# Kernel tuning notes

Hardware: AMD Instinct MI355X
Metric: run time of the kernel (lower is better)

## Reference

```python
import jax, jax.numpy as jnp
import numpy as np

N, S, C, PE, E, L, H = 65536, 128, 128, 8, 262144, 3, 2
NT, ET = 120, 5
EPS_BN = 1e-5


def _bn(x, g, b):
    # training-mode BatchNorm1d over the node dimension
    m = x.mean(axis=0)
    v = x.var(axis=0)
    return (x - m) * jax.lax.rsqrt(v + EPS_BN) * g + b


def _forward(node_type, edge_index, edge_type, pe,
             pe_gamma, pe_beta, pe_W, pe_b, node_emb, edge_emb,
             gine_W1, gine_b1, gine_W2, gine_b2,
             n1_g, n1_b, n2_g, n2_b, n3_g, n3_b,
             attn_inW, attn_inb, attn_outW, attn_outb,
             mlp_W1, mlp_b1, mlp_W2, mlp_b2):
    # input features: [node-type embedding | Linear(BN(pe))]  -> [N, C]
    x = jnp.concatenate([node_emb[node_type],
                         _bn(pe, pe_gamma, pe_beta) @ pe_W + pe_b], axis=1)
    ea = edge_emb[edge_type]            # [E, C], shared across layers
    src, dst = edge_index[0], edge_index[1]
    B = N // S                          # equal-size graphs -> dense batch is a reshape
    hd = C // H
    scale = 1.0 / np.sqrt(hd).astype(np.float32)
    for l in range(L):
        # --- GINEConv (eps=0): gather -> relu(x_j + e_ij) -> scatter-sum -> MLP ---
        msg = jax.nn.relu(x[src] + ea)                       # [E, C]
        agg = jax.ops.segment_sum(msg, dst, num_segments=N)  # [N, C]
        z = x + agg
        h = jax.nn.relu(z @ gine_W1[l] + gine_b1[l]) @ gine_W2[l] + gine_b2[l]
        h = _bn(h + x, n1_g[l], n1_b[l])                     # local branch + residual + BN
        # --- global multi-head self-attention within each graph ---
        xb = x.reshape(B, S, C)
        qkv = xb @ attn_inW[l] + attn_inb[l]                 # [B, S, 3C]
        q, k, v = jnp.split(qkv, 3, axis=-1)
        q = q.reshape(B, S, H, hd)
        k = k.reshape(B, S, H, hd)
        v = v.reshape(B, S, H, hd)
        att = jax.nn.softmax(jnp.einsum('bqhd,bkhd->bhqk', q, k) * scale, axis=-1)
        o = jnp.einsum('bhqk,bkhd->bqhd', att, v).reshape(B, S, C)
        o = (o @ attn_outW[l] + attn_outb[l]).reshape(N, C)
        ha = _bn(o + x, n2_g[l], n2_b[l])                    # attn branch + residual + BN
        # --- combine + FFN ---
        out = h + ha
        out = out + (jax.nn.relu(out @ mlp_W1[l] + mlp_b1[l]) @ mlp_W2[l] + mlp_b2[l])
        x = _bn(out, n3_g[l], n3_b[l])
    return x


def setup_inputs() -> dict:
    keys = iter(jax.random.split(jax.random.key(0), 40))
    nk = lambda: next(keys)
    p = lambda *s: jax.random.normal(nk(), s, jnp.float32) * 0.05
    return {
        'node_type': jax.random.randint(nk(), (N,), 0, NT),
        'pe': jax.random.normal(nk(), (N, 20), jnp.float32),
        'edge_index': jax.random.randint(nk(), (2, E), 0, N),
        'edge_type': jax.random.randint(nk(), (E,), 0, ET),
        'batch': jnp.arange(N) // S,   # 512 equal-size graphs of 128 nodes
        'pe_gamma': jnp.ones(20), 'pe_beta': jnp.zeros(20),
        'pe_W': p(20, PE), 'pe_b': jnp.zeros(PE),
        'node_emb': p(NT, C - PE), 'edge_emb': p(ET, C),
        'gine_W1': p(L, C, C), 'gine_b1': jnp.zeros((L, C)),
        'gine_W2': p(L, C, C), 'gine_b2': jnp.zeros((L, C)),
        'n1_g': jnp.ones((L, C)), 'n1_b': jnp.zeros((L, C)),
        'n2_g': jnp.ones((L, C)), 'n2_b': jnp.zeros((L, C)),
        'n3_g': jnp.ones((L, C)), 'n3_b': jnp.zeros((L, C)),
        'attn_inW': p(L, C, 3 * C), 'attn_inb': jnp.zeros((L, 3 * C)),
        'attn_outW': p(L, C, C), 'attn_outb': jnp.zeros((L, C)),
        'mlp_W1': p(L, C, 2 * C), 'mlp_b1': jnp.zeros((L, 2 * C)),
        'mlp_W2': p(L, 2 * C, C), 'mlp_b2': jnp.zeros((L, C)),
    }


def reference(node_type, pe, edge_index, edge_type, batch,
              pe_gamma, pe_beta, pe_W, pe_b, node_emb, edge_emb,
              gine_W1, gine_b1, gine_W2, gine_b2,
              n1_g, n1_b, n2_g, n2_b, n3_g, n3_b,
              attn_inW, attn_inb, attn_outW, attn_outb,
              mlp_W1, mlp_b1, mlp_W2, mlp_b2):
    # 'batch' is implicit via the equal-size-graph reshape in _forward
    return _forward(node_type, edge_index, edge_type, pe,
                    pe_gamma, pe_beta, pe_W, pe_b, node_emb, edge_emb,
                    gine_W1, gine_b1, gine_W2, gine_b2,
                    n1_g, n1_b, n2_g, n2_b, n3_g, n3_b,
                    attn_inW, attn_inb, attn_outW, attn_outb,
                    mlp_W1, mlp_b1, mlp_W2, mlp_b2)
```

## Files before the change

kernel.cpp:

```cpp
#include <hip/hip_runtime.h>
#include <hip/hip_bf16.h>

#define NN 65536
#define SS 128
#define CC 128
#define EE 262144
#define BB 512
#define LL 3
#define NREP 64

typedef __attribute__((ext_vector_type(8))) short bf16x8;
typedef __attribute__((ext_vector_type(4))) float f32x4;

__device__ __forceinline__ float b2f(unsigned short u) {
    union { unsigned int i; float f; } x; x.i = ((unsigned int)u) << 16; return x.f;
}
__device__ __forceinline__ unsigned short f2b(float f) {
    union { float f; unsigned int i; } x; x.f = f;
    unsigned int r = x.i + 0x7fffu + ((x.i >> 16) & 1u);
    return (unsigned short)(r >> 16);
}
#define SWB(row, colbyte, ROWB) ((row) * (ROWB) + ((colbyte) ^ (((row) & 7) << 4)))

__global__ __launch_bounds__(256) void hist_k(const int* __restrict__ eidx, int* __restrict__ cnt) {
    const int e = blockIdx.x * 256 + threadIdx.x;
    atomicAdd(&cnt[eidx[EE + e]], 1);
}
__global__ __launch_bounds__(256) void scan1_k(const int* __restrict__ cnt, int* __restrict__ row,
                                               int* __restrict__ part) {
    __shared__ int s[256];
    const int tid = threadIdx.x;
    const int i = blockIdx.x * 256 + tid;
    const int v = cnt[i];
    s[tid] = v;
    __syncthreads();
    for (int off = 1; off < 256; off <<= 1) {
        int t = (tid >= off) ? s[tid - off] : 0;
        __syncthreads(); s[tid] += t; __syncthreads();
    }
    row[i] = s[tid] - v;
    if (tid == 255) part[blockIdx.x] = s[255];
}
__global__ __launch_bounds__(256) void scan2_k(int* __restrict__ part) {
    __shared__ int s[256];
    const int tid = threadIdx.x;
    const int v = part[tid];
    s[tid] = v;
    __syncthreads();
    for (int off = 1; off < 256; off <<= 1) {
        int t = (tid >= off) ? s[tid - off] : 0;
        __syncthreads(); s[tid] += t; __syncthreads();
    }
    part[tid] = s[tid] - v;
}
__global__ __launch_bounds__(256) void scan3_k(int* __restrict__ row, const int* __restrict__ part) {
    const int i = blockIdx.x * 256 + threadIdx.x;
    row[i] += part[blockIdx.x];
    if (i == 0) row[NN] = EE;
}
__global__ __launch_bounds__(256) void fill_k(const int* __restrict__ eidx, const int* __restrict__ row,
                                              int* __restrict__ cnt, int* __restrict__ elist) {
    const int e = blockIdx.x * 256 + threadIdx.x;
    const int d = eidx[EE + e];
    const int slot = row[d] + atomicAdd(&cnt[d], 1);
    elist[slot] = e;
}

__global__ __launch_bounds__(256) void cvtw(const float* __restrict__ gW1, const float* __restrict__ gW2,
                                            const float* __restrict__ inW, const float* __restrict__ oW,
                                            const float* __restrict__ mW1, const float* __restrict__ mW2,
                                            unsigned short* __restrict__ WB) {
    const int g = blockIdx.x * 256 + threadIdx.x;
    const int l = g / 163840;
    const int r = g % 163840;
    const float* src; int K, Nc, dst, i;
    if (r < 16384)       { src = gW1 + l * 16384; K = 128; Nc = 128; dst = 0;      i = r; }
    else if (r < 32768)  { src = gW2 + l * 16384; K = 128; Nc = 128; dst = 16384;  i = r - 16384; }
    else if (r < 81920)  { src = inW + l * 49152; K = 128; Nc = 384; dst = 32768;  i = r - 32768; }
    else if (r < 98304)  { src = oW  + l * 16384; K = 128; Nc = 128; dst = 81920;  i = r - 81920; }
    else if (r < 131072) { src = mW1 + l * 32768; K = 128; Nc = 256; dst = 98304;  i = r - 98304; }
    else                 { src = mW2 + l * 32768; K = 256; Nc = 128; dst = 131072; i = r - 131072; }
    const int k = i / Nc, c = i % Nc;
    WB[(size_t)l * 163840 + dst + (size_t)c * K + k] = f2b(src[i]);
}

__global__ __launch_bounds__(256) void colstats_pe(const float* __restrict__ pe,
                                                   float* __restrict__ stats) {
    const int r = blockIdx.x * 256 + threadIdx.x;
    const float* p = pe + (size_t)r * 20;
    float v[20];
    *(float4*)&v[0]  = *(const float4*)(p);
    *(float4*)&v[4]  = *(const float4*)(p + 4);
    *(float4*)&v[8]  = *(const float4*)(p + 8);
    *(float4*)&v[12] = *(const float4*)(p + 12);
    *(float4*)&v[16] = *(const float4*)(p + 16);
    float s[20], q[20];
#pragma unroll
    for (int i = 0; i < 20; ++i) { s[i] = v[i]; q[i] = v[i] * v[i]; }
#pragma unroll
    for (int off = 1; off < 64; off <<= 1) {
#pragma unroll
        for (int i = 0; i < 20; ++i) {
            s[i] += __shfl_xor(s[i], off);
            q[i] += __shfl_xor(q[i], off);
        }
    }
    __shared__ float red[4][40];
    const int lane = threadIdx.x & 63, w = threadIdx.x >> 6;
    if (lane == 0) {
#pragma unroll
        for (int i = 0; i < 20; ++i) { red[w][i] = s[i]; red[w][20 + i] = q[i]; }
    }
    __syncthreads();
    if (threadIdx.x < 40) {
        const float t = red[0][threadIdx.x] + red[1][threadIdx.x] +
                        red[2][threadIdx.x] + red[3][threadIdx.x];
        atomicAdd(&stats[threadIdx.x], t);
    }
}

__global__ void bn_finalize(const float* __restrict__ stats, const float* __restrict__ g,
                            const float* __restrict__ b, float* __restrict__ scoff,
                            int ncols, float invn, int nrep) {
    const int c = threadIdx.x;
    if (c < ncols) {
        float s = 0.f, q = 0.f;
#pragma unroll 8
        for (int r = 0; r < nrep; ++r) {
            s += stats[r * 2 * ncols + c];
            q += stats[r * 2 * ncols + ncols + c];
        }
        float m = s * invn;
        float var = q * invn - m * m;
        float rs = rsqrtf(var + 1e-5f);
        float sc = g[c] * rs;
        scoff[c] = sc;
        scoff[ncols + c] = b[c] - m * sc;
    }
}
__global__ __launch_bounds__(256) void bn_apply_b(const float* __restrict__ in,
                                                  const float* __restrict__ scoff,
                                                  unsigned short* __restrict__ out) {
    const size_t g = (size_t)blockIdx.x * 256 + threadIdx.x;
    const int c8 = ((int)g & 15) << 3;
    float4 a0 = *(const float4*)(in + g * 8);
    float4 a1 = *(const float4*)(in + g * 8 + 4);
    float v[8] = {a0.x, a0.y, a0.z, a0.w, a1.x, a1.y, a1.z, a1.w};
    union { uint4 u; unsigned short s[8]; } o;
#pragma unroll
    for (int i = 0; i < 8; ++i) o.s[i] = f2b(v[i] * scoff[c8 + i] + scoff[128 + c8 + i]);
    *(uint4*)(out + g * 8) = o.u;
}
__global__ __launch_bounds__(256) void bn_apply_f(const float* __restrict__ in,
                                                  const float* __restrict__ scoff,
                                                  float* __restrict__ out) {
    const size_t g = (size_t)blockIdx.x * 256 + threadIdx.x;
    const int c8 = ((int)g & 15) << 3;
    float4 a0 = *(const float4*)(in + g * 8);
    float4 a1 = *(const float4*)(in + g * 8 + 4);
    float v[8] = {a0.x, a0.y, a0.z, a0.w, a1.x, a1.y, a1.z, a1.w};
    float4 o0, o1;
    o0.x = v[0] * scoff[c8 + 0] + scoff[128 + c8 + 0];
    o0.y = v[1] * scoff[c8 + 1] + scoff[128 + c8 + 1];
    o0.z = v[2] * scoff[c8 + 2] + scoff[128 + c8 + 2];
    o0.w = v[3] * scoff[c8 + 3] + scoff[128 + c8 + 3];
    o1.x = v[4] * scoff[c8 + 4] + scoff[128 + c8 + 4];
    o1.y = v[5] * scoff[c8 + 5] + scoff[128 + c8 + 5];
    o1.z = v[6] * scoff[c8 + 6] + scoff[128 + c8 + 6];
    o1.w = v[7] * scoff[c8 + 7] + scoff[128 + c8 + 7];
    *(float4*)(out + g * 8) = o0;
    *(float4*)(out + g * 8 + 4) = o1;
}
__global__ __launch_bounds__(256) void combine2(const float* __restrict__ z,
                                                const float* __restrict__ ha,
                                                const float* __restrict__ scoff,
                                                unsigned short* __restrict__ out) {
    const size_t g = (size_t)blockIdx.x * 256 + threadIdx.x;
    const int c8 = ((int)g & 15) << 3;
    float4 a0 = *(const float4*)(z + g * 8);
    float4 a1 = *(const float4*)(z + g * 8 + 4);
    float4 b0 = *(const float4*)(ha + g * 8);
    float4 b1 = *(const float4*)(ha + g * 8 + 4);
    float va[8] = {a0.x, a0.y, a0.z, a0.w, a1.x, a1.y, a1.z, a1.w};
    float vb[8] = {b0.x, b0.y, b0.z, b0.w, b1.x, b1.y, b1.z, b1.w};
    union { uint4 u; unsigned short s[8]; } o;
#pragma unroll
    for (int i = 0; i < 8; ++i) {
        const int c = c8 + i;
        o.s[i] = f2b(va[i] * scoff[c] + scoff[128 + c] +
                     vb[i] * scoff[256 + c] + scoff[384 + c]);
    }
    *(uint4*)(out + g * 8) = o.u;
}

__global__ __launch_bounds__(256) void embed_b(const int* __restrict__ node_type,
                                               const float* __restrict__ pe,
                                               const float* __restrict__ scoff,
                                               const float* __restrict__ peW,
                                               const float* __restrict__ peB,
                                               const float* __restrict__ node_emb,
                                               unsigned short* __restrict__ XB) {
    const int g = blockIdx.x * 256 + threadIdx.x;
    const int n = g >> 4, c8 = (g & 15) << 3;
    float v[8];
    if (c8 < 120) {
        const float4 a = *(const float4*)(node_emb + (size_t)node_type[n] * 120 + c8);
        const float4 b = *(const float4*)(node_emb + (size_t)node_type[n] * 120 + c8 + 4);
        v[0] = a.x; v[1] = a.y; v[2] = a.z; v[3] = a.w;
        v[4] = b.x; v[5] = b.y; v[6] = b.z; v[7] = b.w;
    } else {
#pragma unroll
        for (int j = 0; j < 8; ++j) v[j] = peB[j];
#pragma unroll
        for (int k = 0; k < 20; ++k) {
            const float p = pe[(size_t)n * 20 + k] * scoff[k] + scoff[20 + k];
#pragma unroll
            for (int j = 0; j < 8; ++j) v[j] = fmaf(p, peW[k * 8 + j], v[j]);
        }
    }
    union { uint4 u; unsigned short s[8]; } o;
#pragma unroll
    for (int i = 0; i < 8; ++i) o.s[i] = f2b(v[i]);
    *(uint4*)(XB + (size_t)g * 8) = o.u;
}

__global__ __launch_bounds__(256) void gine_gather_b(const unsigned short* __restrict__ XB,
                                                     const int* __restrict__ eidx,
                                                     const int* __restrict__ etype,
                                                     const float* __restrict__ edge_emb,
                                                     const int* __restrict__ row,
                                                     const int* __restrict__ elist,
                                                     unsigned short* __restrict__ Z) {
    const int n = blockIdx.x * 16 + (threadIdx.x >> 4);
    const int c8 = (threadIdx.x & 15) << 3;
    const int beg = row[n], end = row[n + 1];
    union { uint4 u; unsigned short s[8]; } x;
    x.u = *(const uint4*)(XB + (size_t)n * 128 + c8);
    float z[8];
#pragma unroll
    for (int i = 0; i < 8; ++i) z[i] = b2f(x.s[i]);
    for (int j = beg; j < end; ++j) {
        const int e = elist[j];
        const int s = eidx[e];
        const int et = etype[e];
        union { uint4 u; unsigned short s[8]; } xs;
        xs.u = *(const uint4*)(XB + (size_t)s * 128 + c8);
        const float4 e0 = *(const float4*)(edge_emb + (size_t)et * 128 + c8);
        const float4 e1 = *(const float4*)(edge_emb + (size_t)et * 128 + c8 + 4);
        z[0] += fmaxf(b2f(xs.s[0]) + e0.x, 0.f);
        z[1] += fmaxf(b2f(xs.s[1]) + e0.y, 0.f);
        z[2] += fmaxf(b2f(xs.s[2]) + e0.z, 0.f);
        z[3] += fmaxf(b2f(xs.s[3]) + e0.w, 0.f);
        z[4] += fmaxf(b2f(xs.s[4]) + e1.x, 0.f);
        z[5] += fmaxf(b2f(xs.s[5]) + e1.y, 0.f);
        z[6] += fmaxf(b2f(xs.s[6]) + e1.z, 0.f);
        z[7] += fmaxf(b2f(xs.s[7]) + e1.w, 0.f);
    }
    union { uint4 u; unsigned short s[8]; } o;
#pragma unroll
    for (int i = 0; i < 8; ++i) o.s[i] = f2b(z[i]);
    *(uint4*)(Z + (size_t)n * 128 + c8) = o.u;
}

template <int RELU, int RESID, int STATS, int KS, int OUTF>
__global__ __launch_bounds__(256) void gemm_ls(const unsigned short* __restrict__ A,
                                               const unsigned short* __restrict__ WT,
                                               const float* __restrict__ bias,
                                               const unsigned short* __restrict__ resid,
                                               void* __restrict__ outp,
                                               float* __restrict__ stats, int Nw) {
    extern __shared__ __align__(16) char LDSX[];
    const int K = KS * 32;
    const int ROWB = K * 2;
    const int tid = threadIdx.x, lane = tid & 63, w = tid >> 6;
    const int lr = lane & 15, lg = lane >> 4;
    const int bm = blockIdx.x * 128;
    const int bn = blockIdx.y * 128;

#pragma unroll
    for (int i = 0; i < K / 16; ++i) {
        const int c = (i * 256 + tid) * 16;
        const int row = c / ROWB, inrow = c % ROWB;
        *(uint4*)(LDSX + SWB(row, inrow, ROWB)) =
            *(const uint4*)(WT + (size_t)(bn + row) * K + (inrow >> 1));
    }
    bf16x8 af[2][KS];
#pragma unroll
    for (int r = 0; r < 2; ++r)
#pragma unroll
        for (int ks = 0; ks < KS; ++ks)
            af[r][ks] = *(const bf16x8*)(A + (size_t)(bm + w * 32 + r * 16 + lr) * K + ks * 32 + lg * 8);
    float bcol[8];
#pragma unroll
    for (int nt = 0; nt < 8; ++nt) bcol[nt] = bias[bn + nt * 16 + lr];
    __syncthreads();

    f32x4 acc[2][8];
#pragma unroll
    for (int r = 0; r < 2; ++r)
#pragma unroll
        for (int nt = 0; nt < 8; ++nt) acc[r][nt] = (f32x4){0.f, 0.f, 0.f, 0.f};
#pragma unroll
    for (int ks = 0; ks < KS; ++ks) {
        bf16x8 bq[8];
#pragma unroll
        for (int nt = 0; nt < 8; ++nt)
            bq[nt] = *(const bf16x8*)(LDSX + SWB(nt * 16 + lr, ks * 64 + lg * 16, ROWB));
#pragma unroll
        for (int r = 0; r < 2; ++r)
#pragma unroll
            for (int nt = 0; nt < 8; ++nt)
                acc[r][nt] = __builtin_amdgcn_mfma_f32_16x16x32_bf16(af[r][ks], bq[nt], acc[r][nt], 0, 0, 0);
    }
    __syncthreads();

#pragma unroll
    for (int r = 0; r < 2; ++r)
#pragma unroll
        for (int nt = 0; nt < 8; ++nt)
#pragma unroll
            for (int j = 0; j < 4; ++j) {
                float v = acc[r][nt][j] + bcol[nt];
                if (RELU) v = fmaxf(v, 0.f);
                const int rl = w * 32 + r * 16 + lg * 4 + j;
                const int col = nt * 16 + lr;
                if (OUTF) ((float*)LDSX)[rl * 128 + col] = v;
                else ((unsigned short*)LDSX)[rl * 128 + col] = f2b(v);
            }
    __syncthreads();

    if (OUTF) {
        float ssum[4] = {0.f, 0.f, 0.f, 0.f}, ssq[4] = {0.f, 0.f, 0.f, 0.f};
#pragma unroll
        for (int i = 0; i < 16; ++i) {
            const int L = (i * 256 + tid) * 16;
            const int row = L >> 9, col = (L & 511) >> 2;
            float4 v = *(const float4*)(LDSX + L);
            if (RESID) {
                const uint2 rv = *(const uint2*)(resid + (size_t)(bm + row) * Nw + bn + col);
                v.x += b2f((unsigned short)(rv.x & 0xffffu));
                v.y += b2f((unsigned short)(rv.x >> 16));
                v.z += b2f((unsigned short)(rv.y & 0xffffu));
                v.w += b2f((unsigned short)(rv.y >> 16));
            }
            if (STATS) {
                ssum[0] += v.x; ssq[0] += v.x * v.x;
                ssum[1] += v.y; ssq[1] += v.y * v.y;
                ssum[2] += v.z; ssq[2] += v.z * v.z;
                ssum[3] += v.w; ssq[3] += v.w * v.w;
            }
            *(float4*)((float*)outp + (size_t)(bm + row) * Nw + bn + col) = v;
        }
        if (STATS) {
#pragma unroll
            for (int c2 = 0; c2 < 4; ++c2) {
                ssum[c2] += __shfl_xor(ssum[c2], 32);
                ssq[c2]  += __shfl_xor(ssq[c2], 32);
            }
            if (lane < 32) {
                float* st = stats + (size_t)(blockIdx.x & (NREP - 1)) * 256;
                const int c0 = (lane & 31) * 4;
#pragma unroll
                for (int c2 = 0; c2 < 4; ++c2) {
                    atomicAdd(&st[c0 + c2], ssum[c2]);
                    atomicAdd(&st[128 + c0 + c2], ssq[c2]);
                }
            }
        }
    } else {
#pragma unroll
        for (int i = 0; i < 8; ++i) {
            const int L = (i * 256 + tid) * 16;
            const int row = L >> 8, colb = L & 255;
            *(uint4*)((char*)outp + ((size_t)(bm + row) * Nw + bn) * 2 + colb) = *(const uint4*)(LDSX + L);
        }
    }
}

__global__ __launch_bounds__(256) void attn_mfma(const unsigned short* __restrict__ R,
                                                 unsigned short* __restrict__ O) {
    __shared__ __align__(16) unsigned short SH[128 * 128];
    __shared__ __align__(16) unsigned short Vp[128 * 72];
    __shared__ float inv[128];
    const int b = blockIdx.x >> 1, h = blockIdx.x & 1;
    const int tid = threadIdx.x, lane = tid & 63, w = tid >> 6;
    const int lr = lane & 15, lg = lane >> 4;
    unsigned short* Qs = SH;
    unsigned short* Ks = SH + 128 * 64;
    const size_t rb = (size_t)b * 128 * 384 + h * 64;
#pragma unroll
    for (int i = 0; i < 4; ++i) {
        const int f = tid + i * 256;
        const int r = f >> 3, ch = f & 7;
        *(uint4*)((char*)Qs + SWB(r, ch * 16, 128)) = *(const uint4*)(R + rb + (size_t)r * 384 + ch * 8);
        *(uint4*)((char*)Ks + SWB(r, ch * 16, 128)) = *(const uint4*)(R + rb + (size_t)r * 384 + 128 + ch * 8);
        *(uint4*)((char*)Vp + r * 144 + ch * 16) = *(const uint4*)(R + rb + (size_t)r * 384 + 256 + ch * 8);
    }
    __syncthreads();
    f32x4 s[8][2];
#pragma unroll
    for (int m = 0; m < 8; ++m)
#pragma unroll
        for (int n = 0; n < 2; ++n) s[m][n] = (f32x4){0.f, 0.f, 0.f, 0.f};
#pragma unroll
    for (int kd = 0; kd < 2; ++kd) {
        bf16x8 ak[8], bq[2];
#pragma unroll
        for (int m = 0; m < 8; ++m)
            ak[m] = *(const bf16x8*)((const char*)Ks + SWB(m * 16 + lr, kd * 64 + lg * 16, 128));
#pragma unroll
        for (int n = 0; n < 2; ++n)
            bq[n] = *(const bf16x8*)((const char*)Qs + SWB(w * 32 + n * 16 + lr, kd * 64 + lg * 16, 128));
#pragma unroll
        for (int m = 0; m < 8; ++m)
#pragma unroll
            for (int n = 0; n < 2; ++n)
                s[m][n] = __builtin_amdgcn_mfma_f32_16x16x32_bf16(ak[m], bq[n], s[m][n], 0, 0, 0);
    }
    const float SC = 0.125f * 1.44269504f;
#pragma unroll
    for (int n = 0; n < 2; ++n) {
        float mx = -1e30f;
#pragma unroll
        for (int m = 0; m < 8; ++m)
#pragma unroll
            for (int j = 0; j < 4; ++j) { s[m][n][j] *= SC; mx = fmaxf(mx, s[m][n][j]); }
        mx = fmaxf(mx, __shfl_xor(mx, 16));
        mx = fmaxf(mx, __shfl_xor(mx, 32));
        float sum = 0.f;
#pragma unroll
        for (int m = 0; m < 8; ++m)
#pragma unroll
            for (int j = 0; j < 4; ++j) {
                const float p = exp2f(s[m][n][j] - mx);
                s[m][n][j] = p;
                sum += p;
            }
        sum += __shfl_xor(sum, 16);
        sum += __shfl_xor(sum, 32);
        if (lg == 0) inv[w * 32 + n * 16 + lr] = 1.0f / sum;
    }
    __syncthreads();
#pragma unroll
    for (int n = 0; n < 2; ++n) {
        const int q = w * 32 + n * 16 + lr;
#pragma unroll
        for (int m = 0; m < 8; ++m) {
            ushort4 pk;
            pk.x = f2b(s[m][n][0]); pk.y = f2b(s[m][n][1]);
            pk.z = f2b(s[m][n][2]); pk.w = f2b(s[m][n][3]);
            *(ushort4*)((char*)SH + SWB(q, (m * 16 + lg * 4) * 2, 256)) = pk;
        }
    }
    __syncthreads();
    f32x4 o[2][4];
#pragma unroll
    for (int m = 0; m < 2; ++m)
#pragma unroll
        for (int n = 0; n < 4; ++n) o[m][n] = (f32x4){0.f, 0.f, 0.f, 0.f};
#pragma unroll
    for (int ks = 0; ks < 4; ++ks) {
        bf16x8 ap[2], bv[4];
#pragma unroll
        for (int m = 0; m < 2; ++m)
            ap[m] = *(const bf16x8*)((const char*)SH + SWB(w * 32 + m * 16 + lr, ks * 64 + lg * 16, 256));
#pragma unroll
        for (int n = 0; n < 4; ++n) {
            union { bf16x8 v; unsigned short u[8]; } t;
#pragma unroll
            for (int i = 0; i < 8; ++i) t.u[i] = Vp[(ks * 32 + lg * 8 + i) * 72 + n * 16 + lr];
            bv[n] = t.v;
        }
#pragma unroll
        for (int m = 0; m < 2; ++m)
#pragma unroll
            for (int n = 0; n < 4; ++n)
                o[m][n] = __builtin_amdgcn_mfma_f32_16x16x32_bf16(ap[m], bv[n], o[m][n], 0, 0, 0);
    }
    __syncthreads();
    unsigned short* Os = SH;
#pragma unroll
    for (int m = 0; m < 2; ++m)
#pragma unroll
        for (int j = 0; j < 4; ++j) {
            const int q = w * 32 + m * 16 + lg * 4 + j;
            const float sc = inv[q];
#pragma unroll
            for (int n = 0; n < 4; ++n)
                Os[q * 64 + n * 16 + lr] = f2b(o[m][n][j] * sc);
        }
    __syncthreads();
#pragma unroll
    for (int i = 0; i < 4; ++i) {
        const int L = (i * 256 + tid) * 16;
        const int row = L >> 7, colb = L & 127;
        *(uint4*)((char*)O + ((size_t)(b * 128 + row) * 128 + h * 64) * 2 + colb) =
            *(const uint4*)((const char*)Os + L);
    }
}

extern "C" void kernel_launch(void* const* d_in, const int* in_sizes, int n_in,
                              void* d_out, int out_size, void* d_ws, size_t ws_size,
                              hipStream_t stream) {
    const int* node_type = (const int*)d_in[0];
    const float* pe = (const float*)d_in[1];
    const int* eidx = (const int*)d_in[2];
    const int* etype = (const int*)d_in[3];
    const float* pe_gamma = (const float*)d_in[5];
    const float* pe_beta = (const float*)d_in[6];
    const float* pe_W = (const float*)d_in[7];
    const float* pe_b = (const float*)d_in[8];
    const float* node_emb = (const float*)d_in[9];
    const float* edge_emb = (const float*)d_in[10];
    const float* gine_W1 = (const float*)d_in[11];
    const float* gine_b1 = (const float*)d_in[12];
    const float* gine_W2 = (const float*)d_in[13];
    const float* gine_b2 = (const float*)d_in[14];
    const float* n1_g = (const float*)d_in[15];
    const float* n1_b = (const float*)d_in[16];
    const float* n2_g = (const float*)d_in[17];
    const float* n2_b = (const float*)d_in[18];
    const float* n3_g = (const float*)d_in[19];
    const float* n3_b = (const float*)d_in[20];
    const float* attn_inW = (const float*)d_in[21];
    const float* attn_inb = (const float*)d_in[22];
    const float* attn_outW = (const float*)d_in[23];
    const float* attn_outb = (const float*)d_in[24];
    const float* mlp_W1 = (const float*)d_in[25];
    const float* mlp_b1 = (const float*)d_in[26];
    const float* mlp_W2 = (const float*)d_in[27];
    const float* mlp_b2 = (const float*)d_in[28];

    const size_t NC = (size_t)NN * CC;
    unsigned short* XB = (unsigned short*)d_ws;
    unsigned short* Zb = XB + NC;
    unsigned short* T1 = Zb + NC;
    unsigned short* Rq = T1 + NC;
    float* HAf = (float*)Rq;
    unsigned short* OUTb = Rq + 2 * NC;
    unsigned short* T2 = Rq + 3 * NC;
    float* Zf = (float*)(T2 + 2 * NC);
    unsigned short* WB = (unsigned short*)(Zf + NC);
    float* STATS = (float*)(WB + 491520);
    const size_t STSZ = (size_t)NREP * 256;
    float* SCOFF = STATS + 3 * STSZ;
    float* SCPE = SCOFF + 512;
    int* icnt = (int*)(SCPE + 64);
    int* irow = icnt + NN;
    int* ielist = irow + NN + 1;
    int* ipart = ielist + EE;

    const int EW16 = NN * 16 / 256;
    const float invn = 1.f / (float)NN;
    float* outF = (float*)d_out;

    hipMemsetAsync(icnt, 0, NN * sizeof(int), stream);
    hist_k<<<EE / 256, 256, 0, stream>>>(eidx, icnt);
    scan1_k<<<NN / 256, 256, 0, stream>>>(icnt, irow, ipart);
    scan2_k<<<1, 256, 0, stream>>>(ipart);
    scan3_k<<<NN / 256, 256, 0, stream>>>(irow, ipart);
    hipMemsetAsync(icnt, 0, NN * sizeof(int), stream);
    fill_k<<<EE / 256, 256, 0, stream>>>(eidx, irow, icnt, ielist);

    cvtw<<<491520 / 256, 256, 0, stream>>>(gine_W1, gine_W2, attn_inW, attn_outW, mlp_W1, mlp_W2, WB);

    hipMemsetAsync(STATS, 0, 64 * sizeof(float), stream);
    colstats_pe<<<NN / 256, 256, 0, stream>>>(pe, STATS);
    bn_finalize<<<1, 64, 0, stream>>>(STATS, pe_gamma, pe_beta, SCPE, 20, invn, 1);
    embed_b<<<EW16, 256, 0, stream>>>(node_type, pe, SCPE, pe_W, pe_b, node_emb, XB);

    const dim3 gB1(NN / 128, 1), gB2(NN / 128, 2), gB3(NN / 128, 3);
    const size_t LDS_B16 = 32768;
    const size_t LDS_F32 = 65536;
    for (int l = 0; l < LL; ++l) {
        unsigned short* WL = WB + (size_t)l * 163840;
        unsigned short* gW1T = WL;
        unsigned short* gW2T = WL + 16384;
        unsigned short* inWT = WL + 32768;
        unsigned short* oWT = WL + 81920;
        unsigned short* mW1T = WL + 98304;
        unsigned short* mW2T = WL + 131072;
        const float* gb1 = gine_b1 + (size_t)l * CC;
        const float* gb2 = gine_b2 + (size_t)l * CC;
        const float* inb = attn_inb + (size_t)l * 384;
        const float* ob = attn_outb + (size_t)l * CC;
        const float* mb1 = mlp_b1 + (size_t)l * 256;
        const float* mb2 = mlp_b2 + (size_t)l * CC;

        hipMemsetAsync(STATS, 0, 3 * STSZ * sizeof(float), stream);

        gine_gather_b<<<NN / 16, 256, 0, stream>>>(XB, eidx, etype, edge_emb, irow, ielist, Zb);
        gemm_ls<1, 0, 0, 4, 0><<<gB1, 256, LDS_B16, stream>>>(Zb, gW1T, gb1, nullptr, T1, nullptr, 128);
        gemm_ls<0, 1, 1, 4, 1><<<gB1, 256, LDS_F32, stream>>>(T1, gW2T, gb2, XB, Zf, STATS, 128);
        bn_finalize<<<1, 128, 0, stream>>>(STATS, n1_g + l * CC, n1_b + l * CC, SCOFF, 128, invn, NREP);

        gemm_ls<0, 0, 0, 4, 0><<<gB3, 256, LDS_B16, stream>>>(XB, inWT, inb, nullptr, Rq, nullptr, 384);
        attn_mfma<<<BB * 2, 256, 0, stream>>>(Rq, T1);
        gemm_ls<0, 1, 1, 4, 1><<<gB1, 256, LDS_F32, stream>>>(T1, oWT, ob, XB, HAf, STATS + STSZ, 128);
        bn_finalize<<<1, 128, 0, stream>>>(STATS + STSZ, n2_g + l * CC, n2_b + l * CC, SCOFF + 256, 128, invn, NREP);

        combine2<<<EW16, 256, 0, stream>>>(Zf, HAf, SCOFF, OUTb);
        gemm_ls<1, 0, 0, 4, 0><<<gB2, 256, LDS_B16, stream>>>(OUTb, mW1T, mb1, nullptr, T2, nullptr, 256);
        gemm_ls<0, 1, 1, 8, 1><<<gB1, 256, LDS_F32, stream>>>(T2, mW2T, mb2, OUTb, Zf, STATS + 2 * STSZ, 128);
        bn_finalize<<<1, 128, 0, stream>>>(STATS + 2 * STSZ, n3_g + l * CC, n3_b + l * CC, SCOFF, 128, invn, NREP);
        if (l < LL - 1)
            bn_apply_b<<<EW16, 256, 0, stream>>>(Zf, SCOFF, XB);
        else
            bn_apply_f<<<EW16, 256, 0, stream>>>(Zf, SCOFF, outF);
    }
}
```

Baseline: 722.1 us.

## Fuse GINE gather, two MLP GEMMs, residual and BN stats into one kernel

Replaces the separate gather kernel and two GEMM launches with one kernel per 128-node tile. It gathers neighbor messages directly into MFMA A-fragments, runs W1 with ReLU through LDS, then W2 plus residual, and accumulates BatchNorm statistics. This removes the global round trips for Zb and T1 and two launches. The cost is that the gather now runs in only 512 blocks, with each lane walking whole rows serially across four k-slices, which lowers memory-level parallelism for the irregular gather.

```diff
diff --git a/kernel.cpp b/kernel.cpp
--- a/kernel.cpp
+++ b/kernel.cpp
@@ -224,42 +224,179 @@
     *(uint4*)(XB + (size_t)g * 8) = o.u;
 }
 
-__global__ __launch_bounds__(256) void gine_gather_b(const unsigned short* __restrict__ XB,
-                                                     const int* __restrict__ eidx,
-                                                     const int* __restrict__ etype,
-                                                     const float* __restrict__ edge_emb,
-                                                     const int* __restrict__ row,
-                                                     const int* __restrict__ elist,
-                                                     unsigned short* __restrict__ Z) {
-    const int n = blockIdx.x * 16 + (threadIdx.x >> 4);
-    const int c8 = (threadIdx.x & 15) << 3;
-    const int beg = row[n], end = row[n + 1];
-    union { uint4 u; unsigned short s[8]; } x;
-    x.u = *(const uint4*)(XB + (size_t)n * 128 + c8);
-    float z[8];
-#pragma unroll
-    for (int i = 0; i < 8; ++i) z[i] = b2f(x.s[i]);
-    for (int j = beg; j < end; ++j) {
-        const int e = elist[j];
-        const int s = eidx[e];
-        const int et = etype[e];
-        union { uint4 u; unsigned short s[8]; } xs;
-        xs.u = *(const uint4*)(XB + (size_t)s * 128 + c8);
-        const float4 e0 = *(const float4*)(edge_emb + (size_t)et * 128 + c8);
-        const float4 e1 = *(const float4*)(edge_emb + (size_t)et * 128 + c8 + 4);
-        z[0] += fmaxf(b2f(xs.s[0]) + e0.x, 0.f);
-        z[1] += fmaxf(b2f(xs.s[1]) + e0.y, 0.f);
-        z[2] += fmaxf(b2f(xs.s[2]) + e0.z, 0.f);
-        z[3] += fmaxf(b2f(xs.s[3]) + e0.w, 0.f);
-        z[4] += fmaxf(b2f(xs.s[4]) + e1.x, 0.f);
-        z[5] += fmaxf(b2f(xs.s[5]) + e1.y, 0.f);
-        z[6] += fmaxf(b2f(xs.s[6]) + e1.z, 0.f);
-        z[7] += fmaxf(b2f(xs.s[7]) + e1.w, 0.f);
-    }
-    union { uint4 u; unsigned short s[8]; } o;
-#pragma unroll
-    for (int i = 0; i < 8; ++i) o.s[i] = f2b(z[i]);
-    *(uint4*)(Z + (size_t)n * 128 + c8) = o.u;
+__global__ __launch_bounds__(256) void gine_fused(const unsigned short* __restrict__ XB,
+                                                  const int* __restrict__ eidx,
+                                                  const int* __restrict__ etype,
+                                                  const float* __restrict__ edge_emb,
+                                                  const int* __restrict__ irow,
+                                                  const int* __restrict__ elist,
+                                                  const unsigned short* __restrict__ W1T,
+                                                  const float* __restrict__ b1,
+                                                  const unsigned short* __restrict__ W2T,
+                                                  const float* __restrict__ b2,
+                                                  float* __restrict__ outp,
+                                                  float* __restrict__ stats) {
+    extern __shared__ __align__(16) char LDSX[];
+    char* slotB = LDSX;
+    char* slotT = LDSX + 32768;
+    const int tid = threadIdx.x, lane = tid & 63, w = tid >> 6;
+    const int lr = lane & 15, lg = lane >> 4;
+    const int bm = blockIdx.x * 128;
+
+#pragma unroll
+    for (int i = 0; i < 8; ++i) {
+        const int c = (i * 256 + tid) * 16;
+        const int row = c >> 8, inrow = c & 255;
+        *(uint4*)(slotB + SWB(row, inrow, 256)) = *(const uint4*)(W1T + (size_t)row * 128 + (inrow >> 1));
+    }
+    bf16x8 af1[2][4];
+#pragma unroll
+    for (int r = 0; r < 2; ++r) {
+        const int row = bm + w * 32 + r * 16 + lr;
+        float z[4][8];
+#pragma unroll
+        for (int ks = 0; ks < 4; ++ks) {
+            union { uint4 u; unsigned short s[8]; } xv;
+            xv.u = *(const uint4*)(XB + (size_t)row * 128 + ks * 32 + lg * 8);
+#pragma unroll
+            for (int i = 0; i < 8; ++i) z[ks][i] = b2f(xv.s[i]);
+        }
+        const int beg = irow[row], end = irow[row + 1];
+        for (int j = beg; j < end; ++j) {
+            const int e = elist[j];
+            const int src = eidx[e];
+            const int et = etype[e];
+#pragma unroll
+            for (int ks = 0; ks < 4; ++ks) {
+                union { uint4 u; unsigned short s[8]; } xs;
+                xs.u = *(const uint4*)(XB + (size_t)src * 128 + ks * 32 + lg * 8);
+                const float4 e0 = *(const float4*)(edge_emb + (size_t)et * 128 + ks * 32 + lg * 8);
+                const float4 e1 = *(const float4*)(edge_emb + (size_t)et * 128 + ks * 32 + lg * 8 + 4);
+                z[ks][0] += fmaxf(b2f(xs.s[0]) + e0.x, 0.f);
+                z[ks][1] += fmaxf(b2f(xs.s[1]) + e0.y, 0.f);
+                z[ks][2] += fmaxf(b2f(xs.s[2]) + e0.z, 0.f);
+                z[ks][3] += fmaxf(b2f(xs.s[3]) + e0.w, 0.f);
+                z[ks][4] += fmaxf(b2f(xs.s[4]) + e1.x, 0.f);
+                z[ks][5] += fmaxf(b2f(xs.s[5]) + e1.y, 0.f);
+                z[ks][6] += fmaxf(b2f(xs.s[6]) + e1.z, 0.f);
+                z[ks][7] += fmaxf(b2f(xs.s[7]) + e1.w, 0.f);
+            }
+        }
+#pragma unroll
+        for (int ks = 0; ks < 4; ++ks) {
+            union { bf16x8 v; unsigned short s[8]; } o;
+#pragma unroll
+            for (int i = 0; i < 8; ++i) o.s[i] = f2b(z[ks][i]);
+            af1[r][ks] = o.v;
+        }
+    }
+    float bc1[8];
+#pragma unroll
+    for (int nt = 0; nt < 8; ++nt) bc1[nt] = b1[nt * 16 + lr];
+    __syncthreads();
+
+    f32x4 acc[2][8];
+#pragma unroll
+    for (int r = 0; r < 2; ++r)
+#pragma unroll
+        for (int nt = 0; nt < 8; ++nt) acc[r][nt] = (f32x4){0.f, 0.f, 0.f, 0.f};
+#pragma unroll
+    for (int ks = 0; ks < 4; ++ks) {
+        bf16x8 bq[8];
+#pragma unroll
+        for (int nt = 0; nt < 8; ++nt)
+            bq[nt] = *(const bf16x8*)(slotB + SWB(nt * 16 + lr, ks * 64 + lg * 16, 256));
+#pragma unroll
+        for (int r = 0; r < 2; ++r)
+#pragma unroll
+            for (int nt = 0; nt < 8; ++nt)
+                acc[r][nt] = __builtin_amdgcn_mfma_f32_16x16x32_bf16(af1[r][ks], bq[nt], acc[r][nt], 0, 0, 0);
+    }
+#pragma unroll
+    for (int r = 0; r < 2; ++r)
+#pragma unroll
+        for (int nt = 0; nt < 8; ++nt)
+#pragma unroll
+            for (int j = 0; j < 4; ++j) {
+                const float v = fmaxf(acc[r][nt][j] + bc1[nt], 0.f);
+                *(unsigned short*)(slotT + SWB(w * 32 + r * 16 + lg * 4 + j, (nt * 16 + lr) * 2, 256)) = f2b(v);
+            }
+    __syncthreads();
+#pragma unroll
+    for (int i = 0; i < 8; ++i) {
+        const int c = (i * 256 + tid) * 16;
+        const int row = c >> 8, inrow = c & 255;
+        *(uint4*)(slotB + SWB(row, inrow, 256)) = *(const uint4*)(W2T + (size_t)row * 128 + (inrow >> 1));
+    }
+    bf16x8 af2[2][4];
+#pragma unroll
+    for (int r = 0; r < 2; ++r)
+#pragma unroll
+        for (int ks = 0; ks < 4; ++ks)
+            af2[r][ks] = *(const bf16x8*)(slotT + SWB(w * 32 + r * 16 + lr, ks * 64 + lg * 16, 256));
+    float bc2[8];
+#pragma unroll
+    for (int nt = 0; nt < 8; ++nt) bc2[nt] = b2[nt * 16 + lr];
+    __syncthreads();
+
+#pragma unroll
+    for (int r = 0; r < 2; ++r)
+#pragma unroll
+        for (int nt = 0; nt < 8; ++nt) acc[r][nt] = (f32x4){0.f, 0.f, 0.f, 0.f};
+#pragma unroll
+    for (int ks = 0; ks < 4; ++ks) {
+        bf16x8 bq[8];
+#pragma unroll
+        for (int nt = 0; nt < 8; ++nt)
+            bq[nt] = *(const bf16x8*)(slotB + SWB(nt * 16 + lr, ks * 64 + lg * 16, 256));
+#pragma unroll
+        for (int r = 0; r < 2; ++r)
+#pragma unroll
+            for (int nt = 0; nt < 8; ++nt)
+                acc[r][nt] = __builtin_amdgcn_mfma_f32_16x16x32_bf16(af2[r][ks], bq[nt], acc[r][nt], 0, 0, 0);
+    }
+    __syncthreads();
+
+#pragma unroll
+    for (int r = 0; r < 2; ++r)
+#pragma unroll
+        for (int nt = 0; nt < 8; ++nt)
+#pragma unroll
+            for (int j = 0; j < 4; ++j)
+                ((float*)LDSX)[(w * 32 + r * 16 + lg * 4 + j) * 128 + nt * 16 + lr] = acc[r][nt][j] + bc2[nt];
+    __syncthreads();
+
+    float ssum[4] = {0.f, 0.f, 0.f, 0.f}, ssq[4] = {0.f, 0.f, 0.f, 0.f};
+#pragma unroll
+    for (int i = 0; i < 16; ++i) {
+        const int L = (i * 256 + tid) * 16;
+        const int row = L >> 9, col = (L & 511) >> 2;
+        float4 v = *(const float4*)(LDSX + L);
+        const uint2 rv = *(const uint2*)(XB + (size_t)(bm + row) * 128 + col);
+        v.x += b2f((unsigned short)(rv.x & 0xffffu));
+        v.y += b2f((unsigned short)(rv.x >> 16));
+        v.z += b2f((unsigned short)(rv.y & 0xffffu));
+        v.w += b2f((unsigned short)(rv.y >> 16));
+        ssum[0] += v.x; ssq[0] += v.x * v.x;
+        ssum[1] += v.y; ssq[1] += v.y * v.y;
+        ssum[2] += v.z; ssq[2] += v.z * v.z;
+        ssum[3] += v.w; ssq[3] += v.w * v.w;
+        *(float4*)(outp + (size_t)(bm + row) * 128 + col) = v;
+    }
+#pragma unroll
+    for (int c2 = 0; c2 < 4; ++c2) {
+        ssum[c2] += __shfl_xor(ssum[c2], 32);
+        ssq[c2]  += __shfl_xor(ssq[c2], 32);
+    }
+    if (lane < 32) {
+        float* st = stats + (size_t)(blockIdx.x & (NREP - 1)) * 256;
+        const int c0 = (lane & 31) * 4;
+#pragma unroll
+        for (int c2 = 0; c2 < 4; ++c2) {
+            atomicAdd(&st[c0 + c2], ssum[c2]);
+            atomicAdd(&st[128 + c0 + c2], ssq[c2]);
+        }
+    }
 }
 
 template <int RELU, int RESID, int STATS, int KS, int OUTF>
@@ -589,9 +726,8 @@
 
         hipMemsetAsync(STATS, 0, 3 * STSZ * sizeof(float), stream);
 
-        gine_gather_b<<<NN / 16, 256, 0, stream>>>(XB, eidx, etype, edge_emb, irow, ielist, Zb);
-        gemm_ls<1, 0, 0, 4, 0><<<gB1, 256, LDS_B16, stream>>>(Zb, gW1T, gb1, nullptr, T1, nullptr, 128);
-        gemm_ls<0, 1, 1, 4, 1><<<gB1, 256, LDS_F32, stream>>>(T1, gW2T, gb2, XB, Zf, STATS, 128);
+        gine_fused<<<NN / 128, 256, LDS_F32, stream>>>(XB, eidx, etype, edge_emb, irow, ielist,
+                                                       gW1T, gb1, gW2T, gb2, Zf, STATS);
         bn_finalize<<<1, 128, 0, stream>>>(STATS, n1_g + l * CC, n1_b + l * CC, SCOFF, 128, invn, NREP);
 
         gemm_ls<0, 0, 0, 4, 0><<<gB3, 256, LDS_B16, stream>>>(XB, inWT, inb, nullptr, Rq, nullptr, 384);
```

Result: no change. 736.1 us (+1.9%).
